# Performance work log

Hardware: AMD Instinct MI355X
Metric: run time of the kernel (lower is better)

## Reference

```python
import jax, jax.numpy as jnp
import numpy as np

B, D, F, NC, HID, SQ = 4096, 19, 64, 256, 32, 16


def setup_inputs() -> dict:
    key = jax.random.key(0)
    ks = jax.random.split(key, 13)
    u = lambda k, shape, s: jax.random.uniform(k, shape, jnp.float32, -s, s)
    s_proj = 1.0 / np.sqrt(61.0)   # torch Linear default init bound
    s_gcn = 1.0 / np.sqrt(float(HID))  # GCNLayer uses 1/sqrt(weight.size(1))
    s_out = 1.0 / np.sqrt(float(HID))
    s_i1 = 1.0 / np.sqrt(float(D))
    s_i2 = 1.0 / np.sqrt(float(SQ))
    return {
        "x": jax.random.normal(ks[0], (B, D, F), jnp.float32),
        "dc": jax.random.uniform(ks[1], (B, D), jnp.float32),
        "centers": jax.random.normal(ks[2], (NC, 61), jnp.float32),
        "proj_w": u(ks[3], (61, D), s_proj),
        "proj_b": u(ks[4], (D,), s_proj),
        "dc_param": jnp.array(0.05, jnp.float32),
        "center_confidence": jnp.ones((NC, D), jnp.float32),
        "gcn_w": u(ks[5], (D, HID), s_gcn),
        "gcn_b": u(ks[6], (HID,), s_gcn),
        "out_w": u(ks[7], (HID, D), s_out),
        "out_b": u(ks[8], (D,), s_out),
        "imp_w1": u(ks[9], (D, SQ), s_i1),
        "imp_b1": u(ks[10], (SQ,), s_i1),
        "imp_w2": u(ks[11], (SQ, D), s_i2),
        "imp_b2": u(ks[12], (D,), s_i2),
    }


def _adjacency(x_all, dc_all, p):
    # sim_ij = 1 / mean_d[ (1-p)(x_i - x_j)^2 + p * exp(1-dc_i)*exp(1-dc_j) ]
    # Computed without the N x N x d broadcast:
    #   mean_d (x_i - x_j)^2 = (|x_i|^2 + |x_j|^2 - 2 x_i.x_j) / d
    #   mean_d e_i e_j       = (E E^T)_ij / d, e = exp(1 - dc)
    d = x_all.shape[1]
    sq = jnp.sum(x_all * x_all, axis=1)                      # [N]
    sqdist = sq[:, None] + sq[None, :] - 2.0 * (x_all @ x_all.T)  # [N,N]
    e = jnp.exp(1.0 - dc_all)                                # [N,d]
    denom = ((1.0 - p) * sqdist + p * (e @ e.T)) / d
    sim = 1.0 / denom
    n = x_all.shape[0]
    eye = jnp.eye(n, dtype=sim.dtype)
    return sim * (1.0 - eye) + eye


def reference(x, dc, centers, proj_w, proj_b, dc_param, center_confidence,
              gcn_w, gcn_b, out_w, out_b, imp_w1, imp_b1, imp_w2, imp_b2):
    b = x.shape[0]
    x_avg = x.mean(axis=-1)                                  # [b, d]
    centers_p = centers @ proj_w + proj_b                    # [nc, d]
    # torch detaches the concatenated node features / confidences
    x_all = jax.lax.stop_gradient(jnp.concatenate([x_avg, centers_p], axis=0))
    dc_all = jax.lax.stop_gradient(jnp.concatenate([dc, center_confidence], axis=0))
    adj = _adjacency(x_all, dc_all, dc_param)                # [N, N]
    group_label = jnp.argmax(adj[:b, b:], axis=1)            # [b]
    emb = adj @ (x_all @ gcn_w) + gcn_b                      # GCN: [N, hid]
    emb = jax.nn.sigmoid(emb @ out_w + out_b)                # [N, d]
    group_embedding = emb[b:]                                # [nc, d]
    group_patients_embedding = group_embedding[group_label]  # [b, d]
    h = jax.nn.gelu(group_embedding @ imp_w1 + imp_b1, approximate=False)
    scores_per_group = jax.nn.sigmoid(h @ imp_w2 + imp_b2)   # [nc, d]
    group_scores = scores_per_group[group_label]             # [b, d]
    return group_scores, group_embedding, group_patients_embedding, group_label
```

## Files before the change

### kernel.cpp

```cpp
#include <hip/hip_runtime.h>
#include <math.h>

#define BB   4096
#define DD   19
#define FF   64
#define NCC  256
#define HID  32
#define SQQ  16
#define NALL (BB + NCC)
#define XSTR 20

#define OFFD_X   0
#define OFFD_SQ  (NALL * XSTR)
#define ND_TOTAL (OFFD_SQ + NALL)

#define OFF_X   0
#define OFF_SQ  (NALL * XSTR)
#define OFF_S   (OFF_SQ + NALL)
#define OFF_G   (OFF_S + NALL)
#define OFF_GE  (OFF_G + NALL * HID)
#define OFF_SC  (OFF_GE + NCC * DD)

#define OUT_GS  0
#define OUT_GE  (BB * DD)
#define OUT_GPE (OUT_GE + NCC * DD)
#define OUT_GL  (OUT_GPE + BB * DD)

__global__ void k1_xavg(const float* __restrict__ x, float* __restrict__ xall,
                        double* __restrict__ xalld) {
    int t = blockIdx.x * 256 + threadIdx.x;
    if (t >= BB * DD) return;
    int i = t / DD, d = t - i * DD;
    const float4* px = (const float4*)(x + (size_t)t * FF);
    double s = 0.0;
#pragma unroll
    for (int k = 0; k < 16; ++k) {
        float4 v = px[k];
        s += ((double)v.x + (double)v.y) + ((double)v.z + (double)v.w);
    }
    double m = s * (1.0 / 64.0);
    xall[i * XSTR + d]  = (float)m;
    xalld[i * XSTR + d] = m;
    if (d == 0) { xall[i * XSTR + DD] = 0.0f; xalld[i * XSTR + DD] = 0.0; }
}

__global__ void k2_centers(const float* __restrict__ centers, const float* __restrict__ pw,
                           const float* __restrict__ pb, float* __restrict__ xall,
                           double* __restrict__ xalld) {
    int t = blockIdx.x * 256 + threadIdx.x;
    if (t >= NCC * DD) return;
    int c = t / DD, d = t - c * DD;
    const float* cr = centers + c * 61;
    double acc = 0.0;
#pragma unroll
    for (int k = 0; k < 61; ++k) acc = fma((double)cr[k], (double)pw[k * DD + d], acc);
    acc += (double)pb[d];
    int row = BB + c;
    xall[row * XSTR + d]  = (float)acc;
    xalld[row * XSTR + d] = acc;
    if (d == 0) { xall[row * XSTR + DD] = 0.0f; xalld[row * XSTR + DD] = 0.0; }
}

__global__ void k3_stats(const float* __restrict__ xall, const double* __restrict__ xalld,
                         const float* __restrict__ dc, const float* __restrict__ gw,
                         float* __restrict__ sqv, double* __restrict__ sqd,
                         float* __restrict__ Sv, float* __restrict__ G) {
    int t = blockIdx.x * 256 + threadIdx.x;
    if (t >= NALL * HID) return;
    int j = t >> 5, h = t & 31;
    const float* xr = xall + j * XSTR;
    float acc = 0.f;
#pragma unroll
    for (int d = 0; d < DD; ++d) acc = fmaf(xr[d], gw[d * HID + h], acc);
    G[j * HID + h] = acc;
    if (h == 0) {
        float s = 0.f;
#pragma unroll
        for (int d = 0; d < DD; ++d) s = fmaf(xr[d], xr[d], s);
        sqv[j] = s;
    }
    if (h == 1) {
        float s;
        if (j < BB) {
            s = 0.f;
            for (int k = 0; k < DD; ++k) s += expf(1.0f - dc[j * DD + k]);
        } else {
            s = 19.0f;
        }
        Sv[j] = s;
    }
    if (h == 2) {
        const double* xd = xalld + j * XSTR;
        double s = 0.0;
#pragma unroll
        for (int d = 0; d < DD; ++d) s = fma(xd[d], xd[d], s);
        sqd[j] = s;
    }
}

__global__ void __launch_bounds__(256) k4_center_emb(
    const float* __restrict__ xall, const float* __restrict__ sqv, const float* __restrict__ Sv,
    const float* __restrict__ G, const float* __restrict__ pscal,
    const float* __restrict__ gcn_b, const float* __restrict__ out_w, const float* __restrict__ out_b,
    const float* __restrict__ iw1, const float* __restrict__ ib1,
    const float* __restrict__ iw2, const float* __restrict__ ib2,
    float* __restrict__ ge, float* __restrict__ scores, float* __restrict__ out_ge)
{
    const int c = blockIdx.x;
    const int t = threadIdx.x;
    const int row = BB + c;
    const float p = pscal[0];
    const float omp = 1.0f - p;
    const float inv_d = 1.0f / 19.0f;

    const float4* xi4 = (const float4*)(xall + row * XSTR);
    float4 xi0 = xi4[0], xi1 = xi4[1], xi2 = xi4[2], xi3 = xi4[3], xi4v = xi4[4];
    float sqi = sqv[row];

    float4 a4[8];
#pragma unroll
    for (int q = 0; q < 8; ++q) a4[q] = make_float4(0.f, 0.f, 0.f, 0.f);

#pragma unroll 1
    for (int k = 0; k < NALL / 256; ++k) {
        int j = t + k * 256;
        const float4* xj = (const float4*)(xall + j * XSTR);
        float4 b0 = xj[0], b1 = xj[1], b2 = xj[2], b3 = xj[3], b4 = xj[4];
        float4 dv;
        dv.x = xi0.x * b0.x; dv.y = xi0.y * b0.y; dv.z = xi0.z * b0.z; dv.w = xi0.w * b0.w;
        dv.x = fmaf(xi1.x, b1.x, dv.x); dv.y = fmaf(xi1.y, b1.y, dv.y);
        dv.z = fmaf(xi1.z, b1.z, dv.z); dv.w = fmaf(xi1.w, b1.w, dv.w);
        dv.x = fmaf(xi2.x, b2.x, dv.x); dv.y = fmaf(xi2.y, b2.y, dv.y);
        dv.z = fmaf(xi2.z, b2.z, dv.z); dv.w = fmaf(xi2.w, b2.w, dv.w);
        dv.x = fmaf(xi3.x, b3.x, dv.x); dv.y = fmaf(xi3.y, b3.y, dv.y);
        dv.z = fmaf(xi3.z, b3.z, dv.z); dv.w = fmaf(xi3.w, b3.w, dv.w);
        dv.x = fmaf(xi4v.x, b4.x, dv.x); dv.y = fmaf(xi4v.y, b4.y, dv.y);
        dv.z = fmaf(xi4v.z, b4.z, dv.z); dv.w = fmaf(xi4v.w, b4.w, dv.w);
        float dot = (dv.x + dv.y) + (dv.z + dv.w);

        float sqdist = sqi + sqv[j] - 2.0f * dot;
        float denom  = (omp * sqdist + p * Sv[j]) * inv_d;
        float sim    = 1.0f / denom;
        float coeff  = (j == row) ? 1.0f : sim;

        const float4* gj = (const float4*)(G + j * HID);
#pragma unroll
        for (int q = 0; q < 8; ++q) {
            float4 g = gj[q];
            a4[q].x = fmaf(coeff, g.x, a4[q].x);
            a4[q].y = fmaf(coeff, g.y, a4[q].y);
            a4[q].z = fmaf(coeff, g.z, a4[q].z);
            a4[q].w = fmaf(coeff, g.w, a4[q].w);
        }
    }

    __shared__ float part[4][HID];
    __shared__ float zbuf[HID];
    __shared__ float gbuf[DD];
    __shared__ float hbuf[SQQ];
    int lane = t & 63, wv = t >> 6;
#pragma unroll
    for (int q = 0; q < 8; ++q) {
        float4 v = a4[q];
        for (int off = 32; off >= 1; off >>= 1) {
            v.x += __shfl_xor(v.x, off);
            v.y += __shfl_xor(v.y, off);
            v.z += __shfl_xor(v.z, off);
            v.w += __shfl_xor(v.w, off);
        }
        if (lane == 0) {
            part[wv][4 * q + 0] = v.x; part[wv][4 * q + 1] = v.y;
            part[wv][4 * q + 2] = v.z; part[wv][4 * q + 3] = v.w;
        }
    }
    __syncthreads();
    if (t < HID) {
        zbuf[t] = part[0][t] + part[1][t] + part[2][t] + part[3][t] + gcn_b[t];
    }
    __syncthreads();
    if (t < DD) {
        float z = out_b[t];
#pragma unroll
        for (int h = 0; h < HID; ++h) z = fmaf(zbuf[h], out_w[h * DD + t], z);
        float o = 1.0f / (1.0f + expf(-z));
        gbuf[t] = o;
        ge[c * DD + t] = o;
        out_ge[c * DD + t] = o;
    }
    __syncthreads();
    if (t < SQQ) {
        float z = ib1[t];
#pragma unroll
        for (int d = 0; d < DD; ++d) z = fmaf(gbuf[d], iw1[d * SQQ + t], z);
        hbuf[t] = 0.5f * z * (1.0f + erff(z * 0.70710678118654752f));
    }
    __syncthreads();
    if (t < DD) {
        float z = ib2[t];
#pragma unroll
        for (int q = 0; q < SQQ; ++q) z = fmaf(hbuf[q], iw2[q * DD + t], z);
        scores[c * DD + t] = 1.0f / (1.0f + expf(-z));
    }
}

__global__ void __launch_bounds__(256) k5_labels(
    const double* __restrict__ xalld, const double* __restrict__ sqd,
    const float* __restrict__ ge, const float* __restrict__ scores,
    float* __restrict__ out)
{
    __shared__ double cx[NCC][XSTR];
    __shared__ double csq[NCC];
    int t = threadIdx.x;
    {
        const double2* src = (const double2*)(xalld + (size_t)(BB + t) * XSTR);
        double2* dst = (double2*)(&cx[t][0]);
#pragma unroll
        for (int q = 0; q < 10; ++q) dst[q] = src[q];
        csq[t] = sqd[BB + t];
    }
    __syncthreads();

    int lane = t & 63, wv = t >> 6;
    int i = blockIdx.x * 4 + wv;

    double xi[DD];
    const double* xr = xalld + (size_t)i * XSTR;
#pragma unroll
    for (int d = 0; d < DD; ++d) xi[d] = xr[d];

    double best = 1e300; int bi = 0;
#pragma unroll
    for (int k = 0; k < 4; ++k) {
        int c = lane + 64 * k;
        const double* cr = &cx[c][0];
        double dot = 0.0;
#pragma unroll
        for (int d = 0; d < DD; ++d) dot = fma(xi[d], cr[d], dot);
        double cost = csq[c] - 2.0 * dot;
        if (cost < best) { best = cost; bi = c; }
    }
    for (int off = 32; off >= 1; off >>= 1) {
        double ov = __shfl_xor(best, off);
        int    oi = __shfl_xor(bi, off);
        if (ov < best || (ov == best && oi < bi)) { best = ov; bi = oi; }
    }

    if (lane < DD) {
        out[OUT_GS  + (size_t)i * DD + lane] = scores[bi * DD + lane];
        out[OUT_GPE + (size_t)i * DD + lane] = ge[bi * DD + lane];
    }
    if (lane == 0) out[OUT_GL + i] = (float)bi;
}

extern "C" void kernel_launch(void* const* d_in, const int* in_sizes, int n_in,
                              void* d_out, int out_size, void* d_ws, size_t ws_size,
                              hipStream_t stream) {
    const float* x        = (const float*)d_in[0];
    const float* dc       = (const float*)d_in[1];
    const float* centers  = (const float*)d_in[2];
    const float* proj_w   = (const float*)d_in[3];
    const float* proj_b   = (const float*)d_in[4];
    const float* dc_param = (const float*)d_in[5];
    const float* gcn_w    = (const float*)d_in[7];
    const float* gcn_b    = (const float*)d_in[8];
    const float* out_w    = (const float*)d_in[9];
    const float* out_b    = (const float*)d_in[10];
    const float* imp_w1   = (const float*)d_in[11];
    const float* imp_b1   = (const float*)d_in[12];
    const float* imp_w2   = (const float*)d_in[13];
    const float* imp_b2   = (const float*)d_in[14];

    double* wsd   = (double*)d_ws;
    double* xalld = wsd + OFFD_X;
    double* sqd   = wsd + OFFD_SQ;
    float*  fbase = (float*)(wsd + ND_TOTAL);
    float*  xall  = fbase + OFF_X;
    float*  sqv   = fbase + OFF_SQ;
    float*  Sv    = fbase + OFF_S;
    float*  G     = fbase + OFF_G;
    float*  ge    = fbase + OFF_GE;
    float*  sc    = fbase + OFF_SC;
    float*  out   = (float*)d_out;

    hipLaunchKernelGGL(k1_xavg,    dim3((BB * DD + 255) / 256), dim3(256), 0, stream,
                       x, xall, xalld);
    hipLaunchKernelGGL(k2_centers, dim3((NCC * DD + 255) / 256), dim3(256), 0, stream,
                       centers, proj_w, proj_b, xall, xalld);
    hipLaunchKernelGGL(k3_stats,   dim3((NALL * HID) / 256), dim3(256), 0, stream,
                       xall, xalld, dc, gcn_w, sqv, sqd, Sv, G);
    hipLaunchKernelGGL(k4_center_emb, dim3(NCC), dim3(256), 0, stream,
                       xall, sqv, Sv, G, dc_param, gcn_b, out_w, out_b,
                       imp_w1, imp_b1, imp_w2, imp_b2, ge, sc, out + OUT_GE);
    hipLaunchKernelGGL(k5_labels,  dim3(BB / 4), dim3(256), 0, stream,
                       xalld, sqd, ge, sc, out);
}
```

Before: 141.5 us.

## Merge setup kernels, split GCN aggregation across node chunks, batch label argmin

```diff
diff --git a/kernel.cpp b/kernel.cpp
--- a/kernel.cpp
+++ b/kernel.cpp
@@ -10,172 +10,166 @@
 #define NALL (BB + NCC)
 #define XSTR 20
 
+#define JCH   32
+#define NBLK  (NALL / JCH)
+
 #define OFFD_X   0
-#define OFFD_SQ  (NALL * XSTR)
-#define ND_TOTAL (OFFD_SQ + NALL)
-
-#define OFF_X   0
-#define OFF_SQ  (NALL * XSTR)
-#define OFF_S   (OFF_SQ + NALL)
-#define OFF_G   (OFF_S + NALL)
-#define OFF_GE  (OFF_G + NALL * HID)
-#define OFF_SC  (OFF_GE + NCC * DD)
+#define ND_TOTAL (NALL * XSTR)
+
+#define OFF_X    0
+#define OFF_P    (NALL * XSTR)
+#define OFF_GE   (OFF_P + NCC * NBLK * HID)
+#define OFF_SC   (OFF_GE + NCC * DD)
 
 #define OUT_GS  0
 #define OUT_GE  (BB * DD)
 #define OUT_GPE (OUT_GE + NCC * DD)
 #define OUT_GL  (OUT_GPE + BB * DD)
 
-__global__ void k1_xavg(const float* __restrict__ x, float* __restrict__ xall,
-                        double* __restrict__ xalld) {
-    int t = blockIdx.x * 256 + threadIdx.x;
-    if (t >= BB * DD) return;
-    int i = t / DD, d = t - i * DD;
-    const float4* px = (const float4*)(x + (size_t)t * FF);
-    double s = 0.0;
-#pragma unroll
-    for (int k = 0; k < 16; ++k) {
-        float4 v = px[k];
-        s += ((double)v.x + (double)v.y) + ((double)v.z + (double)v.w);
-    }
-    double m = s * (1.0 / 64.0);
-    xall[i * XSTR + d]  = (float)m;
-    xalld[i * XSTR + d] = m;
-    if (d == 0) { xall[i * XSTR + DD] = 0.0f; xalld[i * XSTR + DD] = 0.0; }
-}
-
-__global__ void k2_centers(const float* __restrict__ centers, const float* __restrict__ pw,
-                           const float* __restrict__ pb, float* __restrict__ xall,
-                           double* __restrict__ xalld) {
-    int t = blockIdx.x * 256 + threadIdx.x;
-    if (t >= NCC * DD) return;
-    int c = t / DD, d = t - c * DD;
-    const float* cr = centers + c * 61;
-    double acc = 0.0;
-#pragma unroll
-    for (int k = 0; k < 61; ++k) acc = fma((double)cr[k], (double)pw[k * DD + d], acc);
-    acc += (double)pb[d];
-    int row = BB + c;
-    xall[row * XSTR + d]  = (float)acc;
-    xalld[row * XSTR + d] = acc;
-    if (d == 0) { xall[row * XSTR + DD] = 0.0f; xalld[row * XSTR + DD] = 0.0; }
-}
-
-__global__ void k3_stats(const float* __restrict__ xall, const double* __restrict__ xalld,
-                         const float* __restrict__ dc, const float* __restrict__ gw,
-                         float* __restrict__ sqv, double* __restrict__ sqd,
-                         float* __restrict__ Sv, float* __restrict__ G) {
-    int t = blockIdx.x * 256 + threadIdx.x;
-    if (t >= NALL * HID) return;
-    int j = t >> 5, h = t & 31;
-    const float* xr = xall + j * XSTR;
-    float acc = 0.f;
-#pragma unroll
-    for (int d = 0; d < DD; ++d) acc = fmaf(xr[d], gw[d * HID + h], acc);
-    G[j * HID + h] = acc;
-    if (h == 0) {
+__global__ void k12_build(const float* __restrict__ x, const float* __restrict__ centers,
+                          const float* __restrict__ pw, const float* __restrict__ pb,
+                          float* __restrict__ xall, double* __restrict__ xalld) {
+    int blk = blockIdx.x;
+    int tid = threadIdx.x;
+    if (blk < 304) {
+        int t = blk * 256 + tid;
+        int i = t / DD, d = t - i * DD;
+        const float4* px = (const float4*)(x + (size_t)t * FF);
+        double s = 0.0;
+#pragma unroll
+        for (int k = 0; k < 16; ++k) {
+            float4 v = px[k];
+            s += ((double)v.x + (double)v.y) + ((double)v.z + (double)v.w);
+        }
+        double m = s * (1.0 / 64.0);
+        xall[i * XSTR + d]  = (float)m;
+        xalld[i * XSTR + d] = m;
+        if (d == 0) { xall[i * XSTR + DD] = 0.0f; xalld[i * XSTR + DD] = 0.0; }
+    } else {
+        int t = (blk - 304) * 256 + tid;
+        if (t >= NCC * DD) return;
+        int c = t / DD, d = t - c * DD;
+        const float* cr = centers + c * 61;
+        double acc = 0.0;
+#pragma unroll
+        for (int k = 0; k < 61; ++k) acc = fma((double)cr[k], (double)pw[k * DD + d], acc);
+        acc += (double)pb[d];
+        int row = BB + c;
+        xall[row * XSTR + d]  = (float)acc;
+        xalld[row * XSTR + d] = acc;
+        if (d == 0) { xall[row * XSTR + DD] = 0.0f; xalld[row * XSTR + DD] = 0.0; }
+    }
+}
+
+__global__ void __launch_bounds__(256) k4a_partial(
+    const float* __restrict__ xall, const float* __restrict__ dc,
+    const float* __restrict__ gw, const float* __restrict__ pscal,
+    float* __restrict__ partials)
+{
+    __shared__ float xs[JCH * XSTR];
+    __shared__ float gwS[DD * HID];
+    __shared__ float Gs[JCH * HID];
+    __shared__ float sqS[JCH];
+    __shared__ float Ss[JCH];
+
+    const int blk = blockIdx.x;
+    const int t   = threadIdx.x;
+    const int j0  = blk * JCH;
+
+    if (t < JCH * XSTR / 4) {
+        ((float4*)xs)[t] = ((const float4*)xall)[(size_t)j0 * (XSTR / 4) + t];
+    }
+    if (t < 304) { gwS[t] = gw[t]; int u = t + 304; if (u < DD * HID) gwS[u] = gw[u]; }
+    __syncthreads();
+
+    if (t < JCH) {
         float s = 0.f;
 #pragma unroll
-        for (int d = 0; d < DD; ++d) s = fmaf(xr[d], xr[d], s);
-        sqv[j] = s;
-    }
-    if (h == 1) {
+        for (int d = 0; d < DD; ++d) s = fmaf(xs[t * XSTR + d], xs[t * XSTR + d], s);
+        sqS[t] = s;
+    } else if (t < 2 * JCH) {
+        int r = t - JCH, j = j0 + r;
         float s;
         if (j < BB) {
             s = 0.f;
             for (int k = 0; k < DD; ++k) s += expf(1.0f - dc[j * DD + k]);
-        } else {
-            s = 19.0f;
-        }
-        Sv[j] = s;
-    }
-    if (h == 2) {
-        const double* xd = xalld + j * XSTR;
-        double s = 0.0;
-#pragma unroll
-        for (int d = 0; d < DD; ++d) s = fma(xd[d], xd[d], s);
-        sqd[j] = s;
-    }
-}
-
-__global__ void __launch_bounds__(256) k4_center_emb(
-    const float* __restrict__ xall, const float* __restrict__ sqv, const float* __restrict__ Sv,
-    const float* __restrict__ G, const float* __restrict__ pscal,
-    const float* __restrict__ gcn_b, const float* __restrict__ out_w, const float* __restrict__ out_b,
+        } else s = 19.0f;
+        Ss[r] = s;
+    }
+#pragma unroll
+    for (int q = 0; q < 4; ++q) {
+        int idx = t + 256 * q;
+        int r = idx >> 5, h = idx & 31;
+        float acc = 0.f;
+#pragma unroll
+        for (int d = 0; d < DD; ++d) acc = fmaf(xs[r * XSTR + d], gwS[d * HID + h], acc);
+        Gs[r * HID + h] = acc;
+    }
+
+    const int tc = t;
+    float cr[DD];
+    {
+        const float4* c4 = (const float4*)(xall + (size_t)(BB + tc) * XSTR);
+        float4 a = c4[0], b = c4[1], c = c4[2], d4 = c4[3], e = c4[4];
+        cr[0]=a.x; cr[1]=a.y; cr[2]=a.z; cr[3]=a.w;
+        cr[4]=b.x; cr[5]=b.y; cr[6]=b.z; cr[7]=b.w;
+        cr[8]=c.x; cr[9]=c.y; cr[10]=c.z; cr[11]=c.w;
+        cr[12]=d4.x; cr[13]=d4.y; cr[14]=d4.z; cr[15]=d4.w;
+        cr[16]=e.x; cr[17]=e.y; cr[18]=e.z;
+    }
+    float sqc = 0.f;
+#pragma unroll
+    for (int d = 0; d < DD; ++d) sqc = fmaf(cr[d], cr[d], sqc);
+
+    const float p = pscal[0];
+    const float omp = 1.0f - p;
+    const float inv_d = 1.0f / 19.0f;
+
+    float acc[HID];
+#pragma unroll
+    for (int h = 0; h < HID; ++h) acc[h] = 0.f;
+
+    __syncthreads();
+
+#pragma unroll 1
+    for (int r = 0; r < JCH; ++r) {
+        float dot = 0.f;
+#pragma unroll
+        for (int d = 0; d < DD; ++d) dot = fmaf(cr[d], xs[r * XSTR + d], dot);
+        float sqd_  = sqc + sqS[r] - 2.0f * dot;
+        float denom = (omp * sqd_ + p * Ss[r]) * inv_d;
+        float sim   = 1.0f / denom;
+        float coeff = ((j0 + r) == (BB + tc)) ? 1.0f : sim;
+#pragma unroll
+        for (int h = 0; h < HID; ++h) acc[h] = fmaf(coeff, Gs[r * HID + h], acc[h]);
+    }
+
+    float* dst = partials + ((size_t)tc * NBLK + blk) * HID;
+#pragma unroll
+    for (int q = 0; q < 8; ++q) {
+        ((float4*)dst)[q] = make_float4(acc[4*q], acc[4*q+1], acc[4*q+2], acc[4*q+3]);
+    }
+}
+
+__global__ void __launch_bounds__(64) k4b_epilogue(
+    const float* __restrict__ partials, const float* __restrict__ gcn_b,
+    const float* __restrict__ out_w, const float* __restrict__ out_b,
     const float* __restrict__ iw1, const float* __restrict__ ib1,
     const float* __restrict__ iw2, const float* __restrict__ ib2,
     float* __restrict__ ge, float* __restrict__ scores, float* __restrict__ out_ge)
 {
     const int c = blockIdx.x;
     const int t = threadIdx.x;
-    const int row = BB + c;
-    const float p = pscal[0];
-    const float omp = 1.0f - p;
-    const float inv_d = 1.0f / 19.0f;
-
-    const float4* xi4 = (const float4*)(xall + row * XSTR);
-    float4 xi0 = xi4[0], xi1 = xi4[1], xi2 = xi4[2], xi3 = xi4[3], xi4v = xi4[4];
-    float sqi = sqv[row];
-
-    float4 a4[8];
-#pragma unroll
-    for (int q = 0; q < 8; ++q) a4[q] = make_float4(0.f, 0.f, 0.f, 0.f);
-
-#pragma unroll 1
-    for (int k = 0; k < NALL / 256; ++k) {
-        int j = t + k * 256;
-        const float4* xj = (const float4*)(xall + j * XSTR);
-        float4 b0 = xj[0], b1 = xj[1], b2 = xj[2], b3 = xj[3], b4 = xj[4];
-        float4 dv;
-        dv.x = xi0.x * b0.x; dv.y = xi0.y * b0.y; dv.z = xi0.z * b0.z; dv.w = xi0.w * b0.w;
-        dv.x = fmaf(xi1.x, b1.x, dv.x); dv.y = fmaf(xi1.y, b1.y, dv.y);
-        dv.z = fmaf(xi1.z, b1.z, dv.z); dv.w = fmaf(xi1.w, b1.w, dv.w);
-        dv.x = fmaf(xi2.x, b2.x, dv.x); dv.y = fmaf(xi2.y, b2.y, dv.y);
-        dv.z = fmaf(xi2.z, b2.z, dv.z); dv.w = fmaf(xi2.w, b2.w, dv.w);
-        dv.x = fmaf(xi3.x, b3.x, dv.x); dv.y = fmaf(xi3.y, b3.y, dv.y);
-        dv.z = fmaf(xi3.z, b3.z, dv.z); dv.w = fmaf(xi3.w, b3.w, dv.w);
-        dv.x = fmaf(xi4v.x, b4.x, dv.x); dv.y = fmaf(xi4v.y, b4.y, dv.y);
-        dv.z = fmaf(xi4v.z, b4.z, dv.z); dv.w = fmaf(xi4v.w, b4.w, dv.w);
-        float dot = (dv.x + dv.y) + (dv.z + dv.w);
-
-        float sqdist = sqi + sqv[j] - 2.0f * dot;
-        float denom  = (omp * sqdist + p * Sv[j]) * inv_d;
-        float sim    = 1.0f / denom;
-        float coeff  = (j == row) ? 1.0f : sim;
-
-        const float4* gj = (const float4*)(G + j * HID);
-#pragma unroll
-        for (int q = 0; q < 8; ++q) {
-            float4 g = gj[q];
-            a4[q].x = fmaf(coeff, g.x, a4[q].x);
-            a4[q].y = fmaf(coeff, g.y, a4[q].y);
-            a4[q].z = fmaf(coeff, g.z, a4[q].z);
-            a4[q].w = fmaf(coeff, g.w, a4[q].w);
-        }
-    }
-
-    __shared__ float part[4][HID];
     __shared__ float zbuf[HID];
     __shared__ float gbuf[DD];
     __shared__ float hbuf[SQQ];
-    int lane = t & 63, wv = t >> 6;
-#pragma unroll
-    for (int q = 0; q < 8; ++q) {
-        float4 v = a4[q];
-        for (int off = 32; off >= 1; off >>= 1) {
-            v.x += __shfl_xor(v.x, off);
-            v.y += __shfl_xor(v.y, off);
-            v.z += __shfl_xor(v.z, off);
-            v.w += __shfl_xor(v.w, off);
-        }
-        if (lane == 0) {
-            part[wv][4 * q + 0] = v.x; part[wv][4 * q + 1] = v.y;
-            part[wv][4 * q + 2] = v.z; part[wv][4 * q + 3] = v.w;
-        }
-    }
-    __syncthreads();
+
     if (t < HID) {
-        zbuf[t] = part[0][t] + part[1][t] + part[2][t] + part[3][t] + gcn_b[t];
+        const float* P = partials + (size_t)c * NBLK * HID + t;
+        float s = gcn_b[t];
+#pragma unroll 8
+        for (int b = 0; b < NBLK; ++b) s += P[b * HID];
+        zbuf[t] = s;
     }
     __syncthreads();
     if (t < DD) {
@@ -204,52 +198,78 @@
 }
 
 __global__ void __launch_bounds__(256) k5_labels(
-    const double* __restrict__ xalld, const double* __restrict__ sqd,
+    const double* __restrict__ xalld,
     const float* __restrict__ ge, const float* __restrict__ scores,
     float* __restrict__ out)
 {
-    __shared__ double cx[NCC][XSTR];
+    __shared__ double cxT[DD][NCC];
     __shared__ double csq[NCC];
-    int t = threadIdx.x;
+    __shared__ double px[16][XSTR];
+
+    const int t = threadIdx.x;
+    const int blk = blockIdx.x;
+
     {
-        const double2* src = (const double2*)(xalld + (size_t)(BB + t) * XSTR);
-        double2* dst = (double2*)(&cx[t][0]);
-#pragma unroll
-        for (int q = 0; q < 10; ++q) dst[q] = src[q];
-        csq[t] = sqd[BB + t];
-    }
-    __syncthreads();
-
-    int lane = t & 63, wv = t >> 6;
-    int i = blockIdx.x * 4 + wv;
-
-    double xi[DD];
-    const double* xr = xalld + (size_t)i * XSTR;
-#pragma unroll
-    for (int d = 0; d < DD; ++d) xi[d] = xr[d];
-
-    double best = 1e300; int bi = 0;
-#pragma unroll
-    for (int k = 0; k < 4; ++k) {
-        int c = lane + 64 * k;
-        const double* cr = &cx[c][0];
-        double dot = 0.0;
-#pragma unroll
-        for (int d = 0; d < DD; ++d) dot = fma(xi[d], cr[d], dot);
-        double cost = csq[c] - 2.0 * dot;
-        if (cost < best) { best = cost; bi = c; }
-    }
-    for (int off = 32; off >= 1; off >>= 1) {
-        double ov = __shfl_xor(best, off);
-        int    oi = __shfl_xor(bi, off);
-        if (ov < best || (ov == best && oi < bi)) { best = ov; bi = oi; }
-    }
-
-    if (lane < DD) {
-        out[OUT_GS  + (size_t)i * DD + lane] = scores[bi * DD + lane];
-        out[OUT_GPE + (size_t)i * DD + lane] = ge[bi * DD + lane];
-    }
-    if (lane == 0) out[OUT_GL + i] = (float)bi;
+        const double* src = xalld + (size_t)(BB + t) * XSTR;
+        double s = 0.0;
+#pragma unroll
+        for (int d = 0; d < DD; ++d) {
+            double v = src[d];
+            cxT[d][t] = v;
+            s = fma(v, v, s);
+        }
+        csq[t] = s;
+    }
+    if (t < 160) {
+        int r = t / 10, q = t % 10;
+        const double2* src = (const double2*)(xalld + (size_t)(blk * 16 + r) * XSTR);
+        ((double2*)&px[r][0])[q] = src[q];
+    }
+    __syncthreads();
+
+    const int lane = t & 63, wv = t >> 6;
+
+#pragma unroll 1
+    for (int pp = 0; pp < 2; ++pp) {
+        int pl0 = wv * 4 + pp * 2;
+        int i0 = blk * 16 + pl0;
+        double xi0[DD], xi1[DD];
+#pragma unroll
+        for (int d = 0; d < DD; ++d) { xi0[d] = px[pl0][d]; xi1[d] = px[pl0 + 1][d]; }
+
+        double best0 = 1e300, best1 = 1e300; int bi0 = 0, bi1 = 0;
+#pragma unroll
+        for (int k = 0; k < 4; ++k) {
+            int c = lane + 64 * k;
+            double d0 = 0.0, d1 = 0.0;
+#pragma unroll
+            for (int d = 0; d < DD; ++d) {
+                double v = cxT[d][c];
+                d0 = fma(xi0[d], v, d0);
+                d1 = fma(xi1[d], v, d1);
+            }
+            double cost0 = csq[c] - 2.0 * d0;
+            double cost1 = csq[c] - 2.0 * d1;
+            if (cost0 < best0) { best0 = cost0; bi0 = c; }
+            if (cost1 < best1) { best1 = cost1; bi1 = c; }
+        }
+        for (int off = 32; off >= 1; off >>= 1) {
+            double ov0 = __shfl_xor(best0, off); int oi0 = __shfl_xor(bi0, off);
+            if (ov0 < best0 || (ov0 == best0 && oi0 < bi0)) { best0 = ov0; bi0 = oi0; }
+            double ov1 = __shfl_xor(best1, off); int oi1 = __shfl_xor(bi1, off);
+            if (ov1 < best1 || (ov1 == best1 && oi1 < bi1)) { best1 = ov1; bi1 = oi1; }
+        }
+        if (lane < DD) {
+            out[OUT_GS  + (size_t)i0 * DD + lane]       = scores[bi0 * DD + lane];
+            out[OUT_GPE + (size_t)i0 * DD + lane]       = ge[bi0 * DD + lane];
+            out[OUT_GS  + (size_t)(i0 + 1) * DD + lane] = scores[bi1 * DD + lane];
+            out[OUT_GPE + (size_t)(i0 + 1) * DD + lane] = ge[bi1 * DD + lane];
+        }
+        if (lane == 0) {
+            out[OUT_GL + i0]     = (float)bi0;
+            out[OUT_GL + i0 + 1] = (float)bi1;
+        }
+    }
 }
 
 extern "C" void kernel_launch(void* const* d_in, const int* in_sizes, int n_in,
@@ -272,25 +292,20 @@
 
     double* wsd   = (double*)d_ws;
     double* xalld = wsd + OFFD_X;
-    double* sqd   = wsd + OFFD_SQ;
     float*  fbase = (float*)(wsd + ND_TOTAL);
     float*  xall  = fbase + OFF_X;
-    float*  sqv   = fbase + OFF_SQ;
-    float*  Sv    = fbase + OFF_S;
-    float*  G     = fbase + OFF_G;
-    float*  ge    = fbase + OFF_GE;
+    float*  part  = fbase + OFF_P;
+    float*  geb   = fbase + OFF_GE;
     float*  sc    = fbase + OFF_SC;
     float*  out   = (float*)d_out;
 
-    hipLaunchKernelGGL(k1_xavg,    dim3((BB * DD + 255) / 256), dim3(256), 0, stream,
-                       x, xall, xalld);
-    hipLaunchKernelGGL(k2_centers, dim3((NCC * DD + 255) / 256), dim3(256), 0, stream,
-                       centers, proj_w, proj_b, xall, xalld);
-    hipLaunchKernelGGL(k3_stats,   dim3((NALL * HID) / 256), dim3(256), 0, stream,
-                       xall, xalld, dc, gcn_w, sqv, sqd, Sv, G);
-    hipLaunchKernelGGL(k4_center_emb, dim3(NCC), dim3(256), 0, stream,
-                       xall, sqv, Sv, G, dc_param, gcn_b, out_w, out_b,
-                       imp_w1, imp_b1, imp_w2, imp_b2, ge, sc, out + OUT_GE);
-    hipLaunchKernelGGL(k5_labels,  dim3(BB / 4), dim3(256), 0, stream,
-                       xalld, sqd, ge, sc, out);
-}
+    hipLaunchKernelGGL(k12_build, dim3(304 + 19), dim3(256), 0, stream,
+                       x, centers, proj_w, proj_b, xall, xalld);
+    hipLaunchKernelGGL(k4a_partial, dim3(NBLK), dim3(256), 0, stream,
+                       xall, dc, gcn_w, dc_param, part);
+    hipLaunchKernelGGL(k4b_epilogue, dim3(NCC), dim3(64), 0, stream,
+                       part, gcn_b, out_w, out_b, imp_w1, imp_b1, imp_w2, imp_b2,
+                       geb, sc, out + OUT_GE);
+    hipLaunchKernelGGL(k5_labels, dim3(NCC), dim3(256), 0, stream,
+                       xalld, geb, sc, out);
+}
```

Result: faster. 129.8 us (-8.2%).
